# Kernel tuning notes

Hardware: AMD Instinct MI355X
Metric: run time of the kernel (lower is better)

The kernel has to match this reference:

```python
import jax, jax.numpy as jnp
import numpy as np

IN_CHANNELS = 64
OUT_CHANNELS = 32
X_MIN = -1.0
X_MAX = 1.0


def setup_inputs() -> dict:
    key = jax.random.key(0)
    x = jax.random.normal(key, (8, IN_CHANNELS, 56, 56), dtype=jnp.float32)
    # reset_parameters: linspace over [x_min, x_max] with out_channels+1 knots,
    # left_bounds = knots[:-1], right_bounds = knots[1:], tiled over in_channels.
    domain = jnp.linspace(X_MIN, X_MAX, OUT_CHANNELS + 1, dtype=jnp.float32)
    left_bounds = jnp.tile(domain[:-1].reshape(1, 1, 1, -1), (IN_CHANNELS, 1, 1, 1))
    right_bounds = jnp.tile(domain[1:].reshape(1, 1, 1, -1), (IN_CHANNELS, 1, 1, 1))
    return {"x": x, "left_bounds": left_bounds, "right_bounds": right_bounds}


def reference(x, left_bounds, right_bounds):
    # x: (N, C_in, H, W); bounds: (C_in, 1, 1, C_out)
    xe = x[:, :, :, :, None]                      # (N, C_in, H, W, 1) -> broadcast over C_out
    lb = left_bounds[None]                        # (1, C_in, 1, 1, C_out)
    rb = right_bounds[None]
    norm_const = 4.0 / (rb - lb) ** 2
    # relu(hardtanh(v, x_min, x_max)) == relu(clip(v, x_min, x_max))
    left = jax.nn.relu(jnp.clip(xe - lb, X_MIN, X_MAX))
    right = jax.nn.relu(jnp.clip(rb - xe, X_MIN, X_MAX))
    basis = (left * right * norm_const) ** 2      # (N, C_in, H, W, C_out)
    out = basis.sum(axis=1)                       # (N, H, W, C_out)
    return jnp.transpose(out, (0, 3, 1, 2))       # (N, C_out, H, W)
```

## Files before the change

### kernel.cpp

```cpp
#include <hip/hip_runtime.h>


#define POS_PER_BLOCK 64
#define BINS 32
#define ROW_STRIDE 33
#define HWSZ 3136
#define HW4 784
#define TILES_PER_IMG 49

__device__ __forceinline__ void scat(float xv, float* __restrict__ row) {
    const float tt = fmaf(xv, 16.f, 16.f);
    const float jf = fminf(fmaxf(floorf(tt), 0.f), 31.f);
    const float lb = fmaf(jf, 0.0625f, -1.f);
    const float rb = lb + 0.0625f;
    const float l  = fmaxf(xv - lb, 0.f);
    const float r  = fmaxf(rb - xv, 0.f);
    const float pr = (l * r) * 1024.f;
    atomicAdd(row + (int)jf, pr * pr);
}

__global__ __launch_bounds__(256) void
local_conv2d_basis_kernel(const float* __restrict__ x, float* __restrict__ out) {
    __shared__ __attribute__((aligned(16))) float acc[POS_PER_BLOCK * ROW_STRIDE];

    const int t    = threadIdx.x;
    const int blk  = blockIdx.x;
    const int b    = blk / TILES_PER_IMG;
    const int hw0  = (blk % TILES_PER_IMG) * POS_PER_BLOCK;
    const int slot = t & 15;
    const int c0   = t >> 4;

    float4* accv = (float4*)acc;
#pragma unroll
    for (int i = t; i < (POS_PER_BLOCK * ROW_STRIDE) / 4; i += 256)
        accv[i] = make_float4(0.f, 0.f, 0.f, 0.f);
    __syncthreads();

    const float4* x4 = (const float4*)x;
    const size_t base = (size_t)(b * 64 + c0) * HW4 + (hw0 >> 2) + slot;
    const float4 v0 = x4[base];
    const float4 v1 = x4[base + 16 * HW4];
    const float4 v2 = x4[base + 32 * HW4];
    const float4 v3 = x4[base + 48 * HW4];

    float* r0 = acc + (4 * slot + 0) * ROW_STRIDE;
    float* r1 = acc + (4 * slot + 1) * ROW_STRIDE;
    float* r2 = acc + (4 * slot + 2) * ROW_STRIDE;
    float* r3 = acc + (4 * slot + 3) * ROW_STRIDE;
    scat(v0.x, r0); scat(v0.y, r1); scat(v0.z, r2); scat(v0.w, r3);
    scat(v1.x, r0); scat(v1.y, r1); scat(v1.z, r2); scat(v1.w, r3);
    scat(v2.x, r0); scat(v2.y, r1); scat(v2.z, r2); scat(v2.w, r3);
    scat(v3.x, r0); scat(v3.y, r1); scat(v3.z, r2); scat(v3.w, r3);
    __syncthreads();

    float4* out4 = (float4*)(out + (size_t)b * (BINS * HWSZ) + hw0);
#pragma unroll
    for (int k = 0; k < 2; ++k) {
        const int idx = k * 256 + t;
        const int j   = idx >> 4;
        const int s   = idx & 15;
        float4 v;
        v.x = acc[(4 * s + 0) * ROW_STRIDE + j];
        v.y = acc[(4 * s + 1) * ROW_STRIDE + j];
        v.z = acc[(4 * s + 2) * ROW_STRIDE + j];
        v.w = acc[(4 * s + 3) * ROW_STRIDE + j];
        out4[(size_t)j * HW4 + s] = v;
    }
}

extern "C" void kernel_launch(void* const* d_in, const int* in_sizes, int n_in,
                              void* d_out, int out_size, void* d_ws, size_t ws_size,
                              hipStream_t stream) {
    const float* x = (const float*)d_in[0];
    float* out = (float*)d_out;
    dim3 grid(8 * TILES_PER_IMG);
    dim3 block(256);
    local_conv2d_basis_kernel<<<grid, block, 0, stream>>>(x, out);
}
```

Baseline: 69.11 us.

## Shrink tile to 16 positions per block and interleave blocks across batch

Result: faster. 67.67 us (-2.1%).

```diff
diff --git a/kernel.cpp b/kernel.cpp
--- a/kernel.cpp
+++ b/kernel.cpp
@@ -1,12 +1,13 @@
 #include <hip/hip_runtime.h>
 
 
-#define POS_PER_BLOCK 64
+#define POS_PER_BLOCK 16
 #define BINS 32
 #define ROW_STRIDE 33
 #define HWSZ 3136
 #define HW4 784
-#define TILES_PER_IMG 49
+#define TILES_PER_IMG 196
+#define NBLOCKS (8 * TILES_PER_IMG)
 
 __device__ __forceinline__ void scat(float xv, float* __restrict__ row) {
     const float tt = fmaf(xv, 16.f, 16.f);
@@ -23,48 +24,37 @@
 local_conv2d_basis_kernel(const float* __restrict__ x, float* __restrict__ out) {
     __shared__ __attribute__((aligned(16))) float acc[POS_PER_BLOCK * ROW_STRIDE];
 
-    const int t    = threadIdx.x;
-    const int blk  = blockIdx.x;
+    const int t = threadIdx.x;
+    const int blk  = ((int)blockIdx.x & 7) * TILES_PER_IMG + ((int)blockIdx.x >> 3);
     const int b    = blk / TILES_PER_IMG;
     const int hw0  = (blk % TILES_PER_IMG) * POS_PER_BLOCK;
-    const int slot = t & 15;
-    const int c0   = t >> 4;
+    const int slot = t & 3;
+    const int c    = t >> 2;
+
+    const float4 v = ((const float4*)x)[(size_t)(b * 64 + c) * HW4 + (hw0 >> 2) + slot];
 
     float4* accv = (float4*)acc;
-#pragma unroll
-    for (int i = t; i < (POS_PER_BLOCK * ROW_STRIDE) / 4; i += 256)
-        accv[i] = make_float4(0.f, 0.f, 0.f, 0.f);
+    if (t < (POS_PER_BLOCK * ROW_STRIDE) / 4)
+        accv[t] = make_float4(0.f, 0.f, 0.f, 0.f);
     __syncthreads();
 
-    const float4* x4 = (const float4*)x;
-    const size_t base = (size_t)(b * 64 + c0) * HW4 + (hw0 >> 2) + slot;
-    const float4 v0 = x4[base];
-    const float4 v1 = x4[base + 16 * HW4];
-    const float4 v2 = x4[base + 32 * HW4];
-    const float4 v3 = x4[base + 48 * HW4];
-
     float* r0 = acc + (4 * slot + 0) * ROW_STRIDE;
-    float* r1 = acc + (4 * slot + 1) * ROW_STRIDE;
-    float* r2 = acc + (4 * slot + 2) * ROW_STRIDE;
-    float* r3 = acc + (4 * slot + 3) * ROW_STRIDE;
-    scat(v0.x, r0); scat(v0.y, r1); scat(v0.z, r2); scat(v0.w, r3);
-    scat(v1.x, r0); scat(v1.y, r1); scat(v1.z, r2); scat(v1.w, r3);
-    scat(v2.x, r0); scat(v2.y, r1); scat(v2.z, r2); scat(v2.w, r3);
-    scat(v3.x, r0); scat(v3.y, r1); scat(v3.z, r2); scat(v3.w, r3);
+    float* r1 = r0 + ROW_STRIDE;
+    float* r2 = r1 + ROW_STRIDE;
+    float* r3 = r2 + ROW_STRIDE;
+    scat(v.x, r0); scat(v.y, r1); scat(v.z, r2); scat(v.w, r3);
     __syncthreads();
 
-    float4* out4 = (float4*)(out + (size_t)b * (BINS * HWSZ) + hw0);
-#pragma unroll
-    for (int k = 0; k < 2; ++k) {
-        const int idx = k * 256 + t;
-        const int j   = idx >> 4;
-        const int s   = idx & 15;
-        float4 v;
-        v.x = acc[(4 * s + 0) * ROW_STRIDE + j];
-        v.y = acc[(4 * s + 1) * ROW_STRIDE + j];
-        v.z = acc[(4 * s + 2) * ROW_STRIDE + j];
-        v.w = acc[(4 * s + 3) * ROW_STRIDE + j];
-        out4[(size_t)j * HW4 + s] = v;
+    if (t < 128) {
+        const int j = t >> 2;
+        const int s = t & 3;
+        float4 o;
+        o.x = acc[(4 * s + 0) * ROW_STRIDE + j];
+        o.y = acc[(4 * s + 1) * ROW_STRIDE + j];
+        o.z = acc[(4 * s + 2) * ROW_STRIDE + j];
+        o.w = acc[(4 * s + 3) * ROW_STRIDE + j];
+        float4* out4 = (float4*)(out + (size_t)b * (BINS * HWSZ) + hw0);
+        out4[(size_t)j * HW4 + s] = o;
     }
 }
 
@@ -73,7 +63,7 @@
                               hipStream_t stream) {
     const float* x = (const float*)d_in[0];
     float* out = (float*)d_out;
-    dim3 grid(8 * TILES_PER_IMG);
+    dim3 grid(NBLOCKS);
     dim3 block(256);
     local_conv2d_basis_kernel<<<grid, block, 0, stream>>>(x, out);
 }
```
